# Kernel optimization log

Measured on AMD Instinct MI355X. Metric: run time of the kernel, lower is better.

Reference implementation:

```python
import jax, jax.numpy as jnp
import numpy as np

N, D_IN, D_C, D_Q, K = 4096, 64, 32, 128, 3


def setup_inputs() -> dict:
    key = jax.random.key(0)
    ks = jax.random.split(key, 16)
    rn = lambda k, shp, s: jax.random.normal(k, shp, dtype=jnp.float32) * s
    inp = {
        "x": rn(ks[0], (N, D_IN), 1.0),
        "comms": rn(ks[1], (N, D_C), 0.1),
        # dense positive transition matrix (all entries nonzero -> the
        # trans==0 -> -inf masking step is a faithful no-op here)
        "trans": jax.random.uniform(ks[2], (N, N), dtype=jnp.float32, minval=0.01, maxval=1.0),
        "mask": jnp.ones((N,), dtype=jnp.int32),
        # encoding: Linear(num_inputs + comm_channels, ch_q)
        "W_enc": rn(ks[3], (D_IN + D_C, D_Q), 1.0 / np.sqrt(D_IN + D_C)),
        "b_enc": rn(ks[4], (D_Q,), 0.01),
        # att_decoding[k]: Linear(ch_q, ch_q)
        "W_ad": rn(ks[5], (K, D_Q, D_Q), 1.0 / np.sqrt(D_Q)),
        "b_ad": rn(ks[6], (K, D_Q), 0.01),
        # att[k]: Linear(2*ch_q, 1)
        "w_att": rn(ks[7], (K, 2 * D_Q), 1.0 / np.sqrt(2 * D_Q)),
        "b_att": rn(ks[8], (K,), 0.01),
        # att_vectors[k]: Linear(ch_q, ch_q)
        "W_av": rn(ks[9], (K, D_Q, D_Q), 1.0 / np.sqrt(D_Q)),
        "b_av": rn(ks[10], (K, D_Q), 0.01),
        # decoding: Linear(ch_q, 1)
        "W_dec": rn(ks[11], (D_Q,), 1.0 / np.sqrt(D_Q)),
        "b_dec": rn(ks[12], (), 0.01),
    }
    return inp


def reference(x, comms, trans, mask, W_enc, b_enc, W_ad, b_ad, w_att, b_att,
              W_av, b_av, W_dec, b_dec):
    dq = W_ad.shape[-1]
    # encoding of [node features, communication vector]
    h = jnp.concatenate([x, comms], axis=-1) @ W_enc + b_enc          # (n, dq)
    # trans.transpose(0,1); zeros -> -inf (additive log-mask)
    tb = trans.T
    tb = jnp.where(tb == 0, -jnp.inf, tb)                              # (n, n)
    for k in range(K):
        att = h @ W_ad[k] + b_ad[k]                                    # (n, dq)
        # concat-GAT score: score[i,j] = w_a . att[j] + w_b . att[i] + b
        # (decomposition of Linear(cat(att_t, att_t^T)) -> avoids n x n x 2dq)
        wa, wb = w_att[k, :dq], w_att[k, dq:]
        score = (att @ wb)[:, None] + (att @ wa)[None, :] + b_att[k]   # (n, n)
        focus = jax.nn.softmax(score + tb, axis=1)                     # (n, n)
        v = h @ W_av[k] + b_av[k]                                      # (n, dq)
        h = focus @ v                                                  # (n, dq)
    out = h @ W_dec + b_dec                                            # (n,)
    # final masking (args.rl = False branch): masked nodes -> -inf
    s = out + jnp.where(mask == 0, -jnp.inf, 0.0).astype(out.dtype)
    return s
```

## Files before the change

### kernel.cpp

```cpp
#include <hip/hip_runtime.h>
#include <math.h>

#define N 4096
#define DQ 128
#define DIN 64
#define DC 32
#define NT 9
#define PST9 144
#define PST1 16
#define NIT 256
#define KB 4
#define SW 8

typedef __attribute__((ext_vector_type(8))) short short8;
typedef __attribute__((ext_vector_type(8))) _Float16 half8;
typedef __attribute__((ext_vector_type(4))) float f32x4;

__device__ __forceinline__ unsigned short f2h(float x) {
  return __builtin_bit_cast(unsigned short, (_Float16)x);
}
__device__ __forceinline__ void async16(unsigned short* lds, const unsigned short* g) {
  __builtin_amdgcn_global_load_lds(
      (const __attribute__((address_space(1))) void*)g,
      (__attribute__((address_space(3))) void*)lds, 16, 0, 0);
}

__global__ __launch_bounds__(256) void kExp(const float* __restrict__ trans,
                                            unsigned short* __restrict__ Ef) {
  __shared__ float sh[32 * 65];
  const int tid = threadIdx.x;
  const int ig = blockIdx.x;
  const int kt = blockIdx.y;
  const int r = tid >> 3;
  const int c8 = (tid & 7) * 8;
  const float* src = &trans[((size_t)kt * 32 + r) * N + ig * 64 + c8];
  const float4 v0 = *(const float4*)src;
  const float4 v1 = *(const float4*)(src + 4);
  float* d = &sh[r * 65 + c8];
  d[0] = __expf(v0.x); d[1] = __expf(v0.y); d[2] = __expf(v0.z); d[3] = __expf(v0.w);
  d[4] = __expf(v1.x); d[5] = __expf(v1.y); d[6] = __expf(v1.z); d[7] = __expf(v1.w);
  __syncthreads();
  const int itl = tid >> 6;
  const int lane = tid & 63;
  const int quad = lane >> 4, l15 = lane & 15;
  const int col = itl * 16 + l15;
  unsigned short hb[8];
#pragma unroll
  for (int jj = 0; jj < 8; ++jj) hb[jj] = f2h(sh[(quad * 8 + jj) * 65 + col]);
  const short8 s = {(short)hb[0], (short)hb[1], (short)hb[2], (short)hb[3],
                    (short)hb[4], (short)hb[5], (short)hb[6], (short)hb[7]};
  *(short8*)(Ef + (((size_t)kt * NIT + ig * 4 + itl) * 64 + lane) * 8) = s;
}

__device__ __forceinline__ void v_phase(const float* hs_row, float p,
    const float* __restrict__ W_av_k, const float* __restrict__ b_av_k,
    int r, int d4, unsigned short* shh) {
  float a[4] = {b_av_k[d4], b_av_k[d4 + 1], b_av_k[d4 + 2], b_av_k[d4 + 3]};
  for (int c = 0; c < DQ; ++c) {
    const float hv = hs_row[c];
    const float4 w = *(const float4*)&W_av_k[c * DQ + d4];
    a[0] += hv * w.x; a[1] += hv * w.y; a[2] += hv * w.z; a[3] += hv * w.w;
  }
  const int nt = d4 >> 4;
#pragma unroll
  for (int e = 0; e < 4; ++e)
    shh[nt * 128 + ((d4 + e) & 15) * 8 + r] = f2h(p * a[e]);
  const int c32 = d4 >> 2;
  if (c32 < 16)
    shh[8 * 128 + c32 * 8 + r] = (c32 == 0) ? f2h(p) : 0;
}

__device__ __forceinline__ void v_store(int tid, int blk,
    const unsigned short* shh, unsigned short* __restrict__ Vf) {
  const int kt = blk >> 2, quad = blk & 3;
  if (tid < NT * 16) {
    const int nt = tid >> 4, l15 = tid & 15;
    const size_t dst = (((size_t)kt * NT + nt) * 64 + quad * 16 + l15) * 8;
    *(short8*)(Vf + dst) = *(const short8*)&shh[nt * 128 + l15 * 8];
  }
}

__global__ __launch_bounds__(256) void kVS0(const float* __restrict__ x,
    const float* __restrict__ comms, const float* __restrict__ W_enc,
    const float* __restrict__ b_enc, const float* __restrict__ W_ad_k,
    const float* __restrict__ wa, const float* __restrict__ W_av_k,
    const float* __restrict__ b_av_k, unsigned short* __restrict__ Vf) {
  __shared__ float xs[8][96];
  __shared__ float hs[8][DQ];
  __shared__ float u[DQ];
  __shared__ float pb[8];
  __shared__ __align__(16) unsigned short shh[NT * 128];
  const int tid = threadIdx.x;
  const int blk = blockIdx.x;
  if (tid < 128) {
    const float4 v = *(const float4*)&x[(size_t)blk * 8 * DIN + tid * 4];
    const int idx = tid * 4, r = idx >> 6, c = idx & 63;
    xs[r][c] = v.x; xs[r][c + 1] = v.y; xs[r][c + 2] = v.z; xs[r][c + 3] = v.w;
  } else if (tid < 192) {
    const int t = tid - 128;
    const float4 v = *(const float4*)&comms[(size_t)blk * 8 * DC + t * 4];
    const int idx = t * 4, r = idx >> 5, c = idx & 31;
    xs[r][64 + c] = v.x; xs[r][64 + c + 1] = v.y; xs[r][64 + c + 2] = v.z; xs[r][64 + c + 3] = v.w;
  }
  if (tid < DQ) {
    float s = 0.f;
    const float* wrow = &W_ad_k[tid * DQ];
    for (int q = 0; q < DQ; ++q) s += wrow[q] * wa[q];
    u[tid] = s;
  }
  __syncthreads();
  const int r = tid >> 5;
  const int c32 = tid & 31;
  const int d4 = c32 * 4;
  {
    float a0 = b_enc[d4], a1 = b_enc[d4 + 1], a2 = b_enc[d4 + 2], a3 = b_enc[d4 + 3];
    for (int c = 0; c < 96; ++c) {
      const float hv = xs[r][c];
      const float4 w = *(const float4*)&W_enc[c * DQ + d4];
      a0 += hv * w.x; a1 += hv * w.y; a2 += hv * w.z; a3 += hv * w.w;
    }
    hs[r][d4] = a0; hs[r][d4 + 1] = a1; hs[r][d4 + 2] = a2; hs[r][d4 + 3] = a3;
  }
  __syncthreads();
  float part = 0.f;
  for (int c = c32; c < DQ; c += 32) part += hs[r][c] * u[c];
#pragma unroll
  for (int m = 16; m > 0; m >>= 1) part += __shfl_xor(part, m, 32);
  if (c32 == 0) pb[r] = __expf(part);
  __syncthreads();
  v_phase(hs[r], pb[r], W_av_k, b_av_k, r, d4, shh);
  __syncthreads();
  v_store(tid, blk, shh, Vf);
}

__global__ __launch_bounds__(256) void kVSR(const float* __restrict__ P,
    const float* __restrict__ W_ad_k, const float* __restrict__ wa,
    const float* __restrict__ W_av_k, const float* __restrict__ b_av_k,
    unsigned short* __restrict__ Vf) {
  __shared__ float hs[8][DQ];
  __shared__ float u[DQ];
  __shared__ float pb[8];
  __shared__ __align__(16) unsigned short shh[NT * 128];
  const int tid = threadIdx.x;
  const int r = tid >> 5;
  const int c32 = tid & 31;
  const int d4 = c32 * 4;
  const int j = blockIdx.x * 8 + r;
  if (tid < DQ) {
    float s = 0.f;
    const float* wrow = &W_ad_k[tid * DQ];
    for (int q = 0; q < DQ; ++q) s += wrow[q] * wa[q];
    u[tid] = s;
  }
  float4 num = {0.f, 0.f, 0.f, 0.f};
  float den = 0.f;
#pragma unroll
  for (int s = 0; s < KB; ++s) {
    const float* b = &P[((size_t)s * N + j) * PST9];
    const float4 v = *(const float4*)&b[d4];
    num.x += v.x; num.y += v.y; num.z += v.z; num.w += v.w;
    den += b[128];
  }
  const float inv = 1.f / den;
  hs[r][d4] = num.x * inv; hs[r][d4 + 1] = num.y * inv;
  hs[r][d4 + 2] = num.z * inv; hs[r][d4 + 3] = num.w * inv;
  __syncthreads();
  float part = 0.f;
  for (int c = c32; c < DQ; c += 32) part += hs[r][c] * u[c];
#pragma unroll
  for (int m = 16; m > 0; m >>= 1) part += __shfl_xor(part, m, 32);
  if (c32 == 0) pb[r] = __expf(part);
  __syncthreads();
  v_phase(hs[r], pb[r], W_av_k, b_av_k, r, d4, shh);
  __syncthreads();
  v_store(tid, blockIdx.x, shh, Vf);
}

__global__ __launch_bounds__(256) void kVSRc(const float* __restrict__ P,
    const float* __restrict__ W_ad_k, const float* __restrict__ wa,
    const float* __restrict__ W_av_k, const float* __restrict__ b_av_k,
    const float* __restrict__ W_dec, unsigned short* __restrict__ Vc) {
  __shared__ float hs[8][DQ];
  __shared__ float u[DQ];
  __shared__ float pb[8];
  const int tid = threadIdx.x;
  const int r = tid >> 5;
  const int c32 = tid & 31;
  const int d4 = c32 * 4;
  const int j = blockIdx.x * 8 + r;
  if (tid < DQ) {
    float s = 0.f;
    const float* wrow = &W_ad_k[tid * DQ];
    for (int q = 0; q < DQ; ++q) s += wrow[q] * wa[q];
    u[tid] = s;
  }
  float4 num = {0.f, 0.f, 0.f, 0.f};
  float den = 0.f;
#pragma unroll
  for (int s = 0; s < KB; ++s) {
    const float* b = &P[((size_t)s * N + j) * PST9];
    const float4 v = *(const float4*)&b[d4];
    num.x += v.x; num.y += v.y; num.z += v.z; num.w += v.w;
    den += b[128];
  }
  const float inv = 1.f / den;
  hs[r][d4] = num.x * inv; hs[r][d4 + 1] = num.y * inv;
  hs[r][d4 + 2] = num.z * inv; hs[r][d4 + 3] = num.w * inv;
  __syncthreads();
  float part = 0.f;
  for (int c = c32; c < DQ; c += 32) part += hs[r][c] * u[c];
#pragma unroll
  for (int m = 16; m > 0; m >>= 1) part += __shfl_xor(part, m, 32);
  if (c32 == 0) pb[r] = __expf(part);
  __syncthreads();
  float a[4] = {b_av_k[d4], b_av_k[d4 + 1], b_av_k[d4 + 2], b_av_k[d4 + 3]};
  for (int c = 0; c < DQ; ++c) {
    const float hv = hs[r][c];
    const float4 w = *(const float4*)&W_av_k[c * DQ + d4];
    a[0] += hv * w.x; a[1] += hv * w.y; a[2] += hv * w.z; a[3] += hv * w.w;
  }
  float vd = a[0] * W_dec[d4] + a[1] * W_dec[d4 + 1]
           + a[2] * W_dec[d4 + 2] + a[3] * W_dec[d4 + 3];
#pragma unroll
  for (int m = 16; m > 0; m >>= 1) vd += __shfl_xor(vd, m, 32);
  const float p = pb[r];
  if (c32 < 16) {
    const int blk = blockIdx.x;
    const size_t ix = (((size_t)(blk >> 2)) * 64 + (blk & 3) * 16 + c32) * 8 + r;
    Vc[ix] = (c32 == 0) ? f2h(p * vd) : (c32 == 1) ? f2h(p) : 0;
  }
}

template <int NTT, int PST>
__global__ __launch_bounds__(256) void kGemmR(
    const unsigned short* __restrict__ Ef, const unsigned short* __restrict__ Vf,
    float* __restrict__ P) {
  __shared__ __align__(16) unsigned short lds[4 * 2 * NTT * 512];
  const int tid = threadIdx.x;
  const int w = tid >> 6, lane = tid & 63;
  const int quad = lane >> 4, l15 = lane & 15;
  const int it0 = blockIdx.x * 2;
  const size_t ktw = (size_t)blockIdx.y * (4 * SW) + w * SW;
  unsigned short* myL = lds + w * (2 * NTT * 512);

  f32x4 acc[2][NTT];
#pragma unroll
  for (int ti = 0; ti < 2; ++ti)
#pragma unroll
    for (int nt = 0; nt < NTT; ++nt) acc[ti][nt] = (f32x4){0.f, 0.f, 0.f, 0.f};

#pragma unroll
  for (int c = 0; c < NTT; ++c)
    async16(myL + c * 512, Vf + (ktw * NTT + c) * 512 + lane * 8);
  half8 A0[2], A1[2];
#pragma unroll
  for (int ti = 0; ti < 2; ++ti)
    A0[ti] = __builtin_bit_cast(half8,
        *(const short8*)(Ef + ((ktw * NIT + it0 + ti) * 64 + lane) * 8));

#pragma unroll
  for (int t = 0; t < SW; ++t) {
    if (t + 1 < SW) {
      const size_t ktn = ktw + t + 1;
#pragma unroll
      for (int c = 0; c < NTT; ++c)
        async16(myL + ((t + 1) & 1) * NTT * 512 + c * 512,
                Vf + (ktn * NTT + c) * 512 + lane * 8);
#pragma unroll
      for (int ti = 0; ti < 2; ++ti)
        A1[ti] = __builtin_bit_cast(half8,
            *(const short8*)(Ef + ((ktn * NIT + it0 + ti) * 64 + lane) * 8));
      __builtin_amdgcn_s_waitcnt(0xF70 | (NTT + 2));
    } else {
      __builtin_amdgcn_s_waitcnt(0xF70);
    }
    const unsigned short* bb = myL + (t & 1) * NTT * 512;
#pragma unroll
    for (int nt = 0; nt < NTT; ++nt) {
      const half8 Bh = __builtin_bit_cast(half8,
          *(const short8*)(bb + nt * 512 + lane * 8));
      acc[0][nt] = __builtin_amdgcn_mfma_f32_16x16x32_f16(A0[0], Bh, acc[0][nt], 0, 0, 0);
      acc[1][nt] = __builtin_amdgcn_mfma_f32_16x16x32_f16(A0[1], Bh, acc[1][nt], 0, 0, 0);
    }
    if (t + 1 < SW) { A0[0] = A1[0]; A0[1] = A1[1]; }
  }
  __syncthreads();
  float* lf = (float*)lds;
#pragma unroll
  for (int ti = 0; ti < 2; ++ti)
#pragma unroll
    for (int nt = 0; nt < NTT; ++nt) {
      float4 v; v.x = acc[ti][nt][0]; v.y = acc[ti][nt][1];
      v.z = acc[ti][nt][2]; v.w = acc[ti][nt][3];
      *(float4*)&lf[(w * 2 * NTT + ti * NTT + nt) * 256 + lane * 4] = v;
    }
  __syncthreads();
  float* Pb = P + (size_t)blockIdx.y * N * PST;
  for (int p = w; p < 2 * NTT; p += 4) {
    const int ti = p / NTT, nt = p % NTT;
    float4 s = {0.f, 0.f, 0.f, 0.f};
#pragma unroll
    for (int wv = 0; wv < 4; ++wv) {
      const float4 v = *(const float4*)&lf[(wv * 2 * NTT + p) * 256 + lane * 4];
      s.x += v.x; s.y += v.y; s.z += v.z; s.w += v.w;
    }
    const float sr[4] = {s.x, s.y, s.z, s.w};
    if (NTT == 1 || nt != 8 || l15 == 0) {
#pragma unroll
      for (int r = 0; r < 4; ++r) {
        const int i = (it0 + ti) * 16 + quad * 4 + r;
        Pb[(size_t)i * PST + nt * 16 + l15] = sr[r];
      }
    }
  }
}

__global__ __launch_bounds__(256) void kOut(const float* __restrict__ P3,
    const float* __restrict__ b_dec, const int* __restrict__ mask,
    float* __restrict__ out) {
  const int i = blockIdx.x * 256 + threadIdx.x;
  float num = 0.f, den = 0.f;
#pragma unroll
  for (int s = 0; s < KB; ++s) {
    const float* b = &P3[((size_t)s * N + i) * PST1];
    num += b[0];
    den += b[1];
  }
  out[i] = (mask[i] == 0) ? -INFINITY : num / den + b_dec[0];
}

extern "C" void kernel_launch(void* const* d_in, const int* in_sizes, int n_in,
                              void* d_out, int out_size, void* d_ws, size_t ws_size,
                              hipStream_t stream) {
  (void)in_sizes; (void)n_in; (void)out_size; (void)ws_size;
  const float* x     = (const float*)d_in[0];
  const float* comms = (const float*)d_in[1];
  const float* trans = (const float*)d_in[2];
  const int*   mask  = (const int*)d_in[3];
  const float* W_enc = (const float*)d_in[4];
  const float* b_enc = (const float*)d_in[5];
  const float* W_ad  = (const float*)d_in[6];
  const float* w_att = (const float*)d_in[8];
  const float* W_av  = (const float*)d_in[10];
  const float* b_av  = (const float*)d_in[11];
  const float* W_dec = (const float*)d_in[12];
  const float* b_dec = (const float*)d_in[13];
  float* out         = (float*)d_out;

  char* ws = (char*)d_ws;
  unsigned short* Vf = (unsigned short*)ws;  ws += (size_t)(N / 32) * NT * 512 * 2;
  unsigned short* Vc = (unsigned short*)ws;  ws += (size_t)(N / 32) * 512 * 2;
  unsigned short* Ef = (unsigned short*)ws;  ws += (size_t)N * N * 2;
  float* P  = (float*)ws;                    ws += (size_t)KB * N * PST9 * 4;
  float* P3 = (float*)ws;

  kExp<<<dim3(64, 128), 256, 0, stream>>>(trans, Ef);
  kVS0<<<N / 8, 256, 0, stream>>>(x, comms, W_enc, b_enc, W_ad, w_att,
                                  W_av, b_av, Vf);
  kGemmR<NT, PST9><<<dim3(NIT / 2, KB), 256, 0, stream>>>(Ef, Vf, P);

  kVSR<<<N / 8, 256, 0, stream>>>(P, W_ad + (size_t)1 * DQ * DQ,
                                  w_att + 2 * DQ, W_av + (size_t)1 * DQ * DQ,
                                  b_av + DQ, Vf);
  kGemmR<NT, PST9><<<dim3(NIT / 2, KB), 256, 0, stream>>>(Ef, Vf, P);

  kVSRc<<<N / 8, 256, 0, stream>>>(P, W_ad + (size_t)2 * DQ * DQ,
                                   w_att + 4 * DQ, W_av + (size_t)2 * DQ * DQ,
                                   b_av + 2 * DQ, W_dec, Vc);
  kGemmR<1, PST1><<<dim3(NIT / 2, KB), 256, 0, stream>>>(Ef, Vc, P3);

  kOut<<<N / 256, 256, 0, stream>>>(P3, b_dec, mask, out);
}
```

Baseline: 213.2 us.

## Fuse exp and first V-stage, retile attention GEMMs, fold output into final GEMM

Merges the exp/transpose kernel and the first V-projection kernel into a single launch whose block index selects the role. The 9-tile GEMM now has each block cover 4 row tiles over a shorter K range, and the K split grows from 4 to 8 partial slices. Each loaded V tile is therefore reused across twice as many rows, at the cost of more partial sums and higher register pressure under launch_bounds(256,2). The last single-column GEMM reduces its K-split within one 512-thread block and writes the masked output directly, which removes the P3 buffer and the separate kOut launch.

New measurement: 238.7 us. +11.9%, slower.

```diff
diff --git a/kernel.cpp b/kernel.cpp
--- a/kernel.cpp
+++ b/kernel.cpp
@@ -7,10 +7,8 @@
 #define DC 32
 #define NT 9
 #define PST9 144
-#define PST1 16
 #define NIT 256
-#define KB 4
-#define SW 8
+#define KB2 8
 
 typedef __attribute__((ext_vector_type(8))) short short8;
 typedef __attribute__((ext_vector_type(8))) _Float16 half8;
@@ -23,33 +21,6 @@
   __builtin_amdgcn_global_load_lds(
       (const __attribute__((address_space(1))) void*)g,
       (__attribute__((address_space(3))) void*)lds, 16, 0, 0);
-}
-
-__global__ __launch_bounds__(256) void kExp(const float* __restrict__ trans,
-                                            unsigned short* __restrict__ Ef) {
-  __shared__ float sh[32 * 65];
-  const int tid = threadIdx.x;
-  const int ig = blockIdx.x;
-  const int kt = blockIdx.y;
-  const int r = tid >> 3;
-  const int c8 = (tid & 7) * 8;
-  const float* src = &trans[((size_t)kt * 32 + r) * N + ig * 64 + c8];
-  const float4 v0 = *(const float4*)src;
-  const float4 v1 = *(const float4*)(src + 4);
-  float* d = &sh[r * 65 + c8];
-  d[0] = __expf(v0.x); d[1] = __expf(v0.y); d[2] = __expf(v0.z); d[3] = __expf(v0.w);
-  d[4] = __expf(v1.x); d[5] = __expf(v1.y); d[6] = __expf(v1.z); d[7] = __expf(v1.w);
-  __syncthreads();
-  const int itl = tid >> 6;
-  const int lane = tid & 63;
-  const int quad = lane >> 4, l15 = lane & 15;
-  const int col = itl * 16 + l15;
-  unsigned short hb[8];
-#pragma unroll
-  for (int jj = 0; jj < 8; ++jj) hb[jj] = f2h(sh[(quad * 8 + jj) * 65 + col]);
-  const short8 s = {(short)hb[0], (short)hb[1], (short)hb[2], (short)hb[3],
-                    (short)hb[4], (short)hb[5], (short)hb[6], (short)hb[7]};
-  *(short8*)(Ef + (((size_t)kt * NIT + ig * 4 + itl) * 64 + lane) * 8) = s;
 }
 
 __device__ __forceinline__ void v_phase(const float* hs_row, float p,
@@ -80,57 +51,89 @@
   }
 }
 
-__global__ __launch_bounds__(256) void kVS0(const float* __restrict__ x,
-    const float* __restrict__ comms, const float* __restrict__ W_enc,
-    const float* __restrict__ b_enc, const float* __restrict__ W_ad_k,
-    const float* __restrict__ wa, const float* __restrict__ W_av_k,
-    const float* __restrict__ b_av_k, unsigned short* __restrict__ Vf) {
-  __shared__ float xs[8][96];
-  __shared__ float hs[8][DQ];
-  __shared__ float u[DQ];
-  __shared__ float pb[8];
-  __shared__ __align__(16) unsigned short shh[NT * 128];
+__global__ __launch_bounds__(256) void kExpVS0(const float* __restrict__ trans,
+    unsigned short* __restrict__ Ef,
+    const float* __restrict__ x, const float* __restrict__ comms,
+    const float* __restrict__ W_enc, const float* __restrict__ b_enc,
+    const float* __restrict__ W_ad_k, const float* __restrict__ wa,
+    const float* __restrict__ W_av_k, const float* __restrict__ b_av_k,
+    unsigned short* __restrict__ Vf) {
+  __shared__ __align__(16) char smem[10048];
   const int tid = threadIdx.x;
-  const int blk = blockIdx.x;
-  if (tid < 128) {
-    const float4 v = *(const float4*)&x[(size_t)blk * 8 * DIN + tid * 4];
-    const int idx = tid * 4, r = idx >> 6, c = idx & 63;
-    xs[r][c] = v.x; xs[r][c + 1] = v.y; xs[r][c + 2] = v.z; xs[r][c + 3] = v.w;
-  } else if (tid < 192) {
-    const int t = tid - 128;
-    const float4 v = *(const float4*)&comms[(size_t)blk * 8 * DC + t * 4];
-    const int idx = t * 4, r = idx >> 5, c = idx & 31;
-    xs[r][64 + c] = v.x; xs[r][64 + c + 1] = v.y; xs[r][64 + c + 2] = v.z; xs[r][64 + c + 3] = v.w;
-  }
-  if (tid < DQ) {
-    float s = 0.f;
-    const float* wrow = &W_ad_k[tid * DQ];
-    for (int q = 0; q < DQ; ++q) s += wrow[q] * wa[q];
-    u[tid] = s;
-  }
-  __syncthreads();
-  const int r = tid >> 5;
-  const int c32 = tid & 31;
-  const int d4 = c32 * 4;
-  {
-    float a0 = b_enc[d4], a1 = b_enc[d4 + 1], a2 = b_enc[d4 + 2], a3 = b_enc[d4 + 3];
-    for (int c = 0; c < 96; ++c) {
-      const float hv = xs[r][c];
-      const float4 w = *(const float4*)&W_enc[c * DQ + d4];
-      a0 += hv * w.x; a1 += hv * w.y; a2 += hv * w.z; a3 += hv * w.w;
-    }
-    hs[r][d4] = a0; hs[r][d4 + 1] = a1; hs[r][d4 + 2] = a2; hs[r][d4 + 3] = a3;
-  }
-  __syncthreads();
-  float part = 0.f;
-  for (int c = c32; c < DQ; c += 32) part += hs[r][c] * u[c];
-#pragma unroll
-  for (int m = 16; m > 0; m >>= 1) part += __shfl_xor(part, m, 32);
-  if (c32 == 0) pb[r] = __expf(part);
-  __syncthreads();
-  v_phase(hs[r], pb[r], W_av_k, b_av_k, r, d4, shh);
-  __syncthreads();
-  v_store(tid, blk, shh, Vf);
+  const int bx = blockIdx.x;
+  if (bx < 8192) {
+    float* sh = (float*)smem;
+    const int ig = bx & 63;
+    const int kt = bx >> 6;
+    const int r = tid >> 3;
+    const int c8 = (tid & 7) * 8;
+    const float* src = &trans[((size_t)kt * 32 + r) * N + ig * 64 + c8];
+    const float4 v0 = *(const float4*)src;
+    const float4 v1 = *(const float4*)(src + 4);
+    float* d = &sh[r * 65 + c8];
+    d[0] = __expf(v0.x); d[1] = __expf(v0.y); d[2] = __expf(v0.z); d[3] = __expf(v0.w);
+    d[4] = __expf(v1.x); d[5] = __expf(v1.y); d[6] = __expf(v1.z); d[7] = __expf(v1.w);
+    __syncthreads();
+    const int itl = tid >> 6;
+    const int lane = tid & 63;
+    const int quad = lane >> 4, l15 = lane & 15;
+    const int col = itl * 16 + l15;
+    unsigned short hb[8];
+#pragma unroll
+    for (int jj = 0; jj < 8; ++jj) hb[jj] = f2h(sh[(quad * 8 + jj) * 65 + col]);
+    const short8 s = {(short)hb[0], (short)hb[1], (short)hb[2], (short)hb[3],
+                      (short)hb[4], (short)hb[5], (short)hb[6], (short)hb[7]};
+    *(short8*)(Ef + (((size_t)kt * NIT + ig * 4 + itl) * 64 + lane) * 8) = s;
+  } else {
+    const int blk = bx - 8192;
+    float* xs = (float*)smem;
+    float* hs = (float*)(smem + 3072);
+    float* u  = (float*)(smem + 7168);
+    float* pb = (float*)(smem + 7680);
+    unsigned short* shh = (unsigned short*)(smem + 7712);
+    if (tid < 128) {
+      const float4 v = *(const float4*)&x[(size_t)blk * 8 * DIN + tid * 4];
+      const int idx = tid * 4, r = idx >> 6, c = idx & 63;
+      xs[r * 96 + c] = v.x; xs[r * 96 + c + 1] = v.y;
+      xs[r * 96 + c + 2] = v.z; xs[r * 96 + c + 3] = v.w;
+    } else if (tid < 192) {
+      const int t = tid - 128;
+      const float4 v = *(const float4*)&comms[(size_t)blk * 8 * DC + t * 4];
+      const int idx = t * 4, r = idx >> 5, c = idx & 31;
+      xs[r * 96 + 64 + c] = v.x; xs[r * 96 + 64 + c + 1] = v.y;
+      xs[r * 96 + 64 + c + 2] = v.z; xs[r * 96 + 64 + c + 3] = v.w;
+    }
+    if (tid < DQ) {
+      float s = 0.f;
+      const float* wrow = &W_ad_k[tid * DQ];
+      for (int q = 0; q < DQ; ++q) s += wrow[q] * wa[q];
+      u[tid] = s;
+    }
+    __syncthreads();
+    const int r = tid >> 5;
+    const int c32 = tid & 31;
+    const int d4 = c32 * 4;
+    {
+      float a0 = b_enc[d4], a1 = b_enc[d4 + 1], a2 = b_enc[d4 + 2], a3 = b_enc[d4 + 3];
+      for (int c = 0; c < 96; ++c) {
+        const float hv = xs[r * 96 + c];
+        const float4 w = *(const float4*)&W_enc[c * DQ + d4];
+        a0 += hv * w.x; a1 += hv * w.y; a2 += hv * w.z; a3 += hv * w.w;
+      }
+      hs[r * DQ + d4] = a0; hs[r * DQ + d4 + 1] = a1;
+      hs[r * DQ + d4 + 2] = a2; hs[r * DQ + d4 + 3] = a3;
+    }
+    __syncthreads();
+    float part = 0.f;
+    for (int c = c32; c < DQ; c += 32) part += hs[r * DQ + c] * u[c];
+#pragma unroll
+    for (int m = 16; m > 0; m >>= 1) part += __shfl_xor(part, m, 32);
+    if (c32 == 0) pb[r] = __expf(part);
+    __syncthreads();
+    v_phase(&hs[r * DQ], pb[r], W_av_k, b_av_k, r, d4, shh);
+    __syncthreads();
+    v_store(tid, blk, shh, Vf);
+  }
 }
 
 __global__ __launch_bounds__(256) void kVSR(const float* __restrict__ P,
@@ -155,7 +158,7 @@
   float4 num = {0.f, 0.f, 0.f, 0.f};
   float den = 0.f;
 #pragma unroll
-  for (int s = 0; s < KB; ++s) {
+  for (int s = 0; s < KB2; ++s) {
     const float* b = &P[((size_t)s * N + j) * PST9];
     const float4 v = *(const float4*)&b[d4];
     num.x += v.x; num.y += v.y; num.z += v.z; num.w += v.w;
@@ -197,7 +200,7 @@
   float4 num = {0.f, 0.f, 0.f, 0.f};
   float den = 0.f;
 #pragma unroll
-  for (int s = 0; s < KB; ++s) {
+  for (int s = 0; s < KB2; ++s) {
     const float* b = &P[((size_t)s * N + j) * PST9];
     const float4 v = *(const float4*)&b[d4];
     num.x += v.x; num.y += v.y; num.z += v.z; num.w += v.w;
@@ -231,102 +234,150 @@
   }
 }
 
-template <int NTT, int PST>
-__global__ __launch_bounds__(256) void kGemmR(
+__global__ __launch_bounds__(256, 2) void kGemm9(
     const unsigned short* __restrict__ Ef, const unsigned short* __restrict__ Vf,
     float* __restrict__ P) {
-  __shared__ __align__(16) unsigned short lds[4 * 2 * NTT * 512];
+  __shared__ __align__(16) unsigned short lds[4][2][NT * 512];
   const int tid = threadIdx.x;
   const int w = tid >> 6, lane = tid & 63;
   const int quad = lane >> 4, l15 = lane & 15;
-  const int it0 = blockIdx.x * 2;
-  const size_t ktw = (size_t)blockIdx.y * (4 * SW) + w * SW;
-  unsigned short* myL = lds + w * (2 * NTT * 512);
-
-  f32x4 acc[2][NTT];
-#pragma unroll
-  for (int ti = 0; ti < 2; ++ti)
-#pragma unroll
-    for (int nt = 0; nt < NTT; ++nt) acc[ti][nt] = (f32x4){0.f, 0.f, 0.f, 0.f};
-
-#pragma unroll
-  for (int c = 0; c < NTT; ++c)
-    async16(myL + c * 512, Vf + (ktw * NTT + c) * 512 + lane * 8);
-  half8 A0[2], A1[2];
-#pragma unroll
-  for (int ti = 0; ti < 2; ++ti)
+  const int it0 = blockIdx.x * 4;
+  const size_t ktw = (size_t)blockIdx.y * 16 + w * 4;
+
+  f32x4 acc[4][NT];
+#pragma unroll
+  for (int ti = 0; ti < 4; ++ti)
+#pragma unroll
+    for (int nt = 0; nt < NT; ++nt) acc[ti][nt] = (f32x4){0.f, 0.f, 0.f, 0.f};
+
+#pragma unroll
+  for (int c = 0; c < NT; ++c)
+    async16(&lds[w][0][c * 512], Vf + (ktw * NT + c) * 512 + lane * 8);
+  half8 A0[4], A1[4];
+#pragma unroll
+  for (int ti = 0; ti < 4; ++ti)
     A0[ti] = __builtin_bit_cast(half8,
         *(const short8*)(Ef + ((ktw * NIT + it0 + ti) * 64 + lane) * 8));
 
 #pragma unroll
-  for (int t = 0; t < SW; ++t) {
-    if (t + 1 < SW) {
+  for (int t = 0; t < 4; ++t) {
+    if (t < 3) {
       const size_t ktn = ktw + t + 1;
 #pragma unroll
-      for (int c = 0; c < NTT; ++c)
-        async16(myL + ((t + 1) & 1) * NTT * 512 + c * 512,
-                Vf + (ktn * NTT + c) * 512 + lane * 8);
-#pragma unroll
-      for (int ti = 0; ti < 2; ++ti)
+      for (int c = 0; c < NT; ++c)
+        async16(&lds[w][(t + 1) & 1][c * 512], Vf + (ktn * NT + c) * 512 + lane * 8);
+#pragma unroll
+      for (int ti = 0; ti < 4; ++ti)
         A1[ti] = __builtin_bit_cast(half8,
             *(const short8*)(Ef + ((ktn * NIT + it0 + ti) * 64 + lane) * 8));
-      __builtin_amdgcn_s_waitcnt(0xF70 | (NTT + 2));
+      __builtin_amdgcn_s_waitcnt(0xF70 | (NT + 4));
     } else {
       __builtin_amdgcn_s_waitcnt(0xF70);
     }
-    const unsigned short* bb = myL + (t & 1) * NTT * 512;
-#pragma unroll
-    for (int nt = 0; nt < NTT; ++nt) {
+    const unsigned short* bb = lds[w][t & 1];
+#pragma unroll
+    for (int nt = 0; nt < NT; ++nt) {
       const half8 Bh = __builtin_bit_cast(half8,
           *(const short8*)(bb + nt * 512 + lane * 8));
-      acc[0][nt] = __builtin_amdgcn_mfma_f32_16x16x32_f16(A0[0], Bh, acc[0][nt], 0, 0, 0);
-      acc[1][nt] = __builtin_amdgcn_mfma_f32_16x16x32_f16(A0[1], Bh, acc[1][nt], 0, 0, 0);
-    }
-    if (t + 1 < SW) { A0[0] = A1[0]; A0[1] = A1[1]; }
-  }
-  __syncthreads();
+#pragma unroll
+      for (int ti = 0; ti < 4; ++ti)
+        acc[ti][nt] = __builtin_amdgcn_mfma_f32_16x16x32_f16(A0[ti], Bh, acc[ti][nt], 0, 0, 0);
+    }
+    if (t < 3) {
+#pragma unroll
+      for (int ti = 0; ti < 4; ++ti) A0[ti] = A1[ti];
+    }
+  }
   float* lf = (float*)lds;
-#pragma unroll
-  for (int ti = 0; ti < 2; ++ti)
-#pragma unroll
-    for (int nt = 0; nt < NTT; ++nt) {
-      float4 v; v.x = acc[ti][nt][0]; v.y = acc[ti][nt][1];
-      v.z = acc[ti][nt][2]; v.w = acc[ti][nt][3];
-      *(float4*)&lf[(w * 2 * NTT + ti * NTT + nt) * 256 + lane * 4] = v;
-    }
-  __syncthreads();
-  float* Pb = P + (size_t)blockIdx.y * N * PST;
-  for (int p = w; p < 2 * NTT; p += 4) {
-    const int ti = p / NTT, nt = p % NTT;
-    float4 s = {0.f, 0.f, 0.f, 0.f};
-#pragma unroll
-    for (int wv = 0; wv < 4; ++wv) {
-      const float4 v = *(const float4*)&lf[(wv * 2 * NTT + p) * 256 + lane * 4];
-      s.x += v.x; s.y += v.y; s.z += v.z; s.w += v.w;
-    }
-    const float sr[4] = {s.x, s.y, s.z, s.w};
-    if (NTT == 1 || nt != 8 || l15 == 0) {
-#pragma unroll
-      for (int r = 0; r < 4; ++r) {
-        const int i = (it0 + ti) * 16 + quad * 4 + r;
-        Pb[(size_t)i * PST + nt * 16 + l15] = sr[r];
+  float* Pb = P + (size_t)blockIdx.y * N * PST9;
+#pragma unroll
+  for (int half = 0; half < 2; ++half) {
+    __syncthreads();
+#pragma unroll
+    for (int ti2 = 0; ti2 < 2; ++ti2)
+#pragma unroll
+      for (int nt = 0; nt < NT; ++nt) {
+        const f32x4 a = acc[half * 2 + ti2][nt];
+        float4 v; v.x = a[0]; v.y = a[1]; v.z = a[2]; v.w = a[3];
+        *(float4*)&lf[((w * 2 + ti2) * NT + nt) * 256 + lane * 4] = v;
       }
-    }
-  }
-}
-
-__global__ __launch_bounds__(256) void kOut(const float* __restrict__ P3,
+    __syncthreads();
+    for (int p = w; p < 2 * NT; p += 4) {
+      const int ti2 = p / NT, nt = p % NT;
+      float4 s = {0.f, 0.f, 0.f, 0.f};
+#pragma unroll
+      for (int wv = 0; wv < 4; ++wv) {
+        const float4 v = *(const float4*)&lf[((wv * 2 + ti2) * NT + nt) * 256 + lane * 4];
+        s.x += v.x; s.y += v.y; s.z += v.z; s.w += v.w;
+      }
+      if (nt != 8 || l15 == 0) {
+        const float sr[4] = {s.x, s.y, s.z, s.w};
+#pragma unroll
+        for (int r = 0; r < 4; ++r) {
+          const int i = (it0 + half * 2 + ti2) * 16 + quad * 4 + r;
+          Pb[(size_t)i * PST9 + nt * 16 + l15] = sr[r];
+        }
+      }
+    }
+  }
+}
+
+__global__ __launch_bounds__(512) void kGemmC(
+    const unsigned short* __restrict__ Ef, const unsigned short* __restrict__ Vc,
     const float* __restrict__ b_dec, const int* __restrict__ mask,
     float* __restrict__ out) {
-  const int i = blockIdx.x * 256 + threadIdx.x;
-  float num = 0.f, den = 0.f;
-#pragma unroll
-  for (int s = 0; s < KB; ++s) {
-    const float* b = &P3[((size_t)s * N + i) * PST1];
-    num += b[0];
-    den += b[1];
-  }
-  out[i] = (mask[i] == 0) ? -INFINITY : num / den + b_dec[0];
+  __shared__ __align__(16) unsigned short lds[8][2][512];
+  __shared__ float rf[8][256];
+  __shared__ float nd[2][16];
+  const int tid = threadIdx.x;
+  const int w = tid >> 6, lane = tid & 63;
+  const int quad = lane >> 4, l15 = lane & 15;
+  const int it = blockIdx.x;
+  const size_t ktw = (size_t)w * 16;
+
+  f32x4 acc = {0.f, 0.f, 0.f, 0.f};
+  async16(&lds[w][0][0], Vc + ktw * 512 + lane * 8);
+  half8 A0 = __builtin_bit_cast(half8,
+      *(const short8*)(Ef + ((ktw * NIT + it) * 64 + lane) * 8));
+  half8 A1;
+#pragma unroll
+  for (int t = 0; t < 16; ++t) {
+    if (t < 15) {
+      const size_t ktn = ktw + t + 1;
+      async16(&lds[w][(t + 1) & 1][0], Vc + ktn * 512 + lane * 8);
+      A1 = __builtin_bit_cast(half8,
+          *(const short8*)(Ef + ((ktn * NIT + it) * 64 + lane) * 8));
+      __builtin_amdgcn_s_waitcnt(0xF72);
+    } else {
+      __builtin_amdgcn_s_waitcnt(0xF70);
+    }
+    const half8 Bh = __builtin_bit_cast(half8,
+        *(const short8*)(&lds[w][t & 1][0] + lane * 8));
+    acc = __builtin_amdgcn_mfma_f32_16x16x32_f16(A0, Bh, acc, 0, 0, 0);
+    if (t < 15) A0 = A1;
+  }
+  float4 v; v.x = acc[0]; v.y = acc[1]; v.z = acc[2]; v.w = acc[3];
+  *(float4*)&rf[w][lane * 4] = v;
+  __syncthreads();
+  if (tid < 64) {
+    float s[4];
+#pragma unroll
+    for (int r = 0; r < 4; ++r) {
+      float t = 0.f;
+#pragma unroll
+      for (int wv = 0; wv < 8; ++wv) t += rf[wv][tid * 4 + r];
+      s[r] = t;
+    }
+    if (l15 < 2) {
+#pragma unroll
+      for (int r = 0; r < 4; ++r) nd[l15][quad * 4 + r] = s[r];
+    }
+  }
+  __syncthreads();
+  if (tid < 16) {
+    const int i = it * 16 + tid;
+    out[i] = (mask[i] == 0) ? -INFINITY : nd[0][tid] / nd[1][tid] + b_dec[0];
+  }
 }
 
 extern "C" void kernel_launch(void* const* d_in, const int* in_sizes, int n_in,
@@ -351,23 +402,19 @@
   unsigned short* Vf = (unsigned short*)ws;  ws += (size_t)(N / 32) * NT * 512 * 2;
   unsigned short* Vc = (unsigned short*)ws;  ws += (size_t)(N / 32) * 512 * 2;
   unsigned short* Ef = (unsigned short*)ws;  ws += (size_t)N * N * 2;
-  float* P  = (float*)ws;                    ws += (size_t)KB * N * PST9 * 4;
-  float* P3 = (float*)ws;
-
-  kExp<<<dim3(64, 128), 256, 0, stream>>>(trans, Ef);
-  kVS0<<<N / 8, 256, 0, stream>>>(x, comms, W_enc, b_enc, W_ad, w_att,
-                                  W_av, b_av, Vf);
-  kGemmR<NT, PST9><<<dim3(NIT / 2, KB), 256, 0, stream>>>(Ef, Vf, P);
+  float* P  = (float*)ws;
+
+  kExpVS0<<<8192 + 512, 256, 0, stream>>>(trans, Ef, x, comms, W_enc, b_enc,
+                                          W_ad, w_att, W_av, b_av, Vf);
+  kGemm9<<<dim3(NIT / 4, KB2), 256, 0, stream>>>(Ef, Vf, P);
 
   kVSR<<<N / 8, 256, 0, stream>>>(P, W_ad + (size_t)1 * DQ * DQ,
                                   w_att + 2 * DQ, W_av + (size_t)1 * DQ * DQ,
                                   b_av + DQ, Vf);
-  kGemmR<NT, PST9><<<dim3(NIT / 2, KB), 256, 0, stream>>>(Ef, Vf, P);
+  kGemm9<<<dim3(NIT / 4, KB2), 256, 0, stream>>>(Ef, Vf, P);
 
   kVSRc<<<N / 8, 256, 0, stream>>>(P, W_ad + (size_t)2 * DQ * DQ,
                                    w_att + 4 * DQ, W_av + (size_t)2 * DQ * DQ,
                                    b_av + 2 * DQ, W_dec, Vc);
-  kGemmR<1, PST1><<<dim3(NIT / 2, KB), 256, 0, stream>>>(Ef, Vc, P3);
-
-  kOut<<<N / 256, 256, 0, stream>>>(P3, b_dec, mask, out);
-}
+  kGemmC<<<NIT, 512, 0, stream>>>(Ef, Vc, b_dec, mask, out);
+}
```
